# Kernel tuning notes

Measured on AMD Instinct MI355X. Metric: run time of the kernel, lower is better.

The kernel has to match this reference:

```python
import jax, jax.numpy as jnp
import numpy as np

B, S, D, H = 4, 2048, 1024, 16
HD = D // H

def setup_inputs() -> dict:
    key = jax.random.key(0)
    k1, k2, k3 = jax.random.split(key, 3)
    x = jax.random.normal(k1, (B, S, D), dtype=jnp.float32)
    W_qkv = jax.random.normal(k2, (D, 3 * D), dtype=jnp.float32) * (1.0 / np.sqrt(D))
    W_out = jax.random.normal(k3, (D, D), dtype=jnp.float32) * (1.0 / np.sqrt(D))
    causal_mask = jnp.tril(jnp.ones((S, S), dtype=bool))[None, None]  # [1,1,S,S]
    return {"x": x, "causal_mask": causal_mask, "W_qkv": W_qkv, "W_out": W_out}

def reference(x, causal_mask, W_qkv, W_out):
    b, s, d = x.shape
    scale = 1.0 / np.sqrt(HD)
    qkv = x @ W_qkv  # [b,s,3d]
    q, k, v = jnp.split(qkv, 3, axis=-1)
    # [b,h,s,hd]
    q = q.reshape(b, s, H, HD).transpose(0, 2, 1, 3)
    k = k.reshape(b, s, H, HD).transpose(0, 2, 1, 3)
    v = v.reshape(b, s, H, HD).transpose(0, 2, 1, 3)
    scores = jnp.einsum('bhqd,bhkd->bhqk', q, k) * scale
    scores = jnp.where(causal_mask, scores, -jnp.inf)
    attn = jax.nn.softmax(scores, axis=-1)
    out = jnp.einsum('bhqk,bhkd->bhqd', attn, v)
    out = out.transpose(0, 2, 1, 3).reshape(b, s, d)
    return out @ W_out
```

## Files before the change

kernel.cpp:

```cpp
#include <hip/hip_runtime.h>
#include <hip/hip_bf16.h>

typedef __bf16 bf16;
typedef unsigned short u16;
typedef unsigned int u32;
typedef __attribute__((ext_vector_type(8))) __bf16 bf16x8;
typedef __attribute__((ext_vector_type(4))) unsigned short u16x4;
typedef __attribute__((ext_vector_type(4))) float f32x4;

#define B_  4
#define S_  2048
#define D_  1024
#define H_  16
#define HD_ 64

#define QSCALE 0.18033688f

__device__ inline u16 bf16_bits(float f) {
  bf16 h = (bf16)f;
  return __builtin_bit_cast(u16, h);
}

__device__ __forceinline__ void glds16(const bf16* g, bf16* s) {
  __builtin_amdgcn_global_load_lds(
      (const __attribute__((address_space(1))) void*)g,
      (__attribute__((address_space(3))) void*)s, 16, 0, 0);
}

#define MEMFENCE() asm volatile("" ::: "memory")
#define BARRIER_RAW() __builtin_amdgcn_s_barrier()
#define LGKM0() asm volatile("s_waitcnt lgkmcnt(0)" ::: "memory")
#define VMCNT(n) asm volatile("s_waitcnt vmcnt(" #n ")" ::: "memory")

__global__ void cvt_x(const float* __restrict__ in, bf16* __restrict__ out, long n) {
  long i = ((long)blockIdx.x * 256 + threadIdx.x) * 8;
  if (i < n) {
    f32x4 a = *(const f32x4*)(in + i);
    f32x4 b = *(const f32x4*)(in + i + 4);
    bf16x8 v;
#pragma unroll
    for (int j = 0; j < 4; ++j) { v[j] = (bf16)a[j]; v[4 + j] = (bf16)b[j]; }
    *(bf16x8*)(out + i) = v;
  }
}

__global__ void cvt_w(const float* __restrict__ in, bf16* __restrict__ out,
                      int K, int N) {
  __shared__ float tile[32][33];
  int n0 = blockIdx.x * 32, k0 = blockIdx.y * 32;
  int x = threadIdx.x, y = threadIdx.y;
#pragma unroll
  for (int i = 0; i < 32; i += 8)
    tile[y + i][x] = in[(long)(k0 + y + i) * N + (n0 + x)];
  __syncthreads();
#pragma unroll
  for (int i = 0; i < 32; i += 8)
    out[(long)(n0 + y + i) * K + (k0 + x)] = (bf16)tile[x][y + i];
}

template <typename TC>
__launch_bounds__(256)
__global__ void gemm128(const bf16* __restrict__ A, const bf16* __restrict__ Bt,
                        TC* __restrict__ C, int M, int N, int K) {
  __shared__ __attribute__((aligned(16))) bf16 As[8][512];
  __shared__ __attribute__((aligned(16))) bf16 Bs[8][512];
  int t = threadIdx.x;
  int w = t >> 6, lane = t & 63;
  int wr = w >> 1, wc = w & 1;
  int fr = lane & 15, fq = lane >> 4;
  long m0 = (long)blockIdx.y * 128, n0 = (long)blockIdx.x * 128;
  f32x4 acc[4][4] = {};
  const bf16* ag = A  + (m0 + (2 * w) * 16 + fr) * (long)K + fq * 8;
  const bf16* bg = Bt + (n0 + (2 * w) * 16 + fr) * (long)K + fq * 8;
  bf16* al0 = &As[2 * w][0];
  bf16* al1 = &As[2 * w + 1][0];
  bf16* bl0 = &Bs[2 * w][0];
  bf16* bl1 = &Bs[2 * w + 1][0];
  const long K16 = 16 * (long)K;
  for (int k0 = 0; k0 < K; k0 += 32) {
    __syncthreads();
    glds16(ag + k0, al0);
    glds16(ag + k0 + K16, al1);
    glds16(bg + k0, bl0);
    glds16(bg + k0 + K16, bl1);
    __syncthreads();
    bf16x8 af[4], bfv[4];
#pragma unroll
    for (int i = 0; i < 4; ++i) {
      af[i]  = *(const bf16x8*)&As[wr * 4 + i][lane * 8];
      bfv[i] = *(const bf16x8*)&Bs[wc * 4 + i][lane * 8];
    }
#pragma unroll
    for (int mb = 0; mb < 4; ++mb)
#pragma unroll
      for (int nb = 0; nb < 4; ++nb)
        acc[mb][nb] = __builtin_amdgcn_mfma_f32_16x16x32_bf16(
            af[mb], bfv[nb], acc[mb][nb], 0, 0, 0);
  }
#pragma unroll
  for (int mb = 0; mb < 4; ++mb) {
    long row = m0 + wr * 64 + mb * 16 + fq * 4;
#pragma unroll
    for (int nb = 0; nb < 4; ++nb) {
      long col = n0 + wc * 64 + nb * 16 + fr;
#pragma unroll
      for (int i = 0; i < 4; ++i)
        C[(row + i) * (long)N + col] = (TC)acc[mb][nb][i];
    }
  }
}

#define QUAD3(MH, NH)                                                         \
  do {                                                                        \
    _Pragma("unroll") for (int m2 = 0; m2 < 2; ++m2) {                        \
      _Pragma("unroll") for (int n2 = 0; n2 < 3; ++n2) {                      \
        _Pragma("unroll") for (int kc = 0; kc < 2; ++kc)                      \
            acc[(MH) * 2 + m2][(NH) * 3 + n2] =                               \
                __builtin_amdgcn_mfma_f32_16x16x32_bf16(                      \
                    aF[m2][kc], bF[(NH) * 3 + n2][kc],                        \
                    acc[(MH) * 2 + m2][(NH) * 3 + n2], 0, 0, 0);              \
      }                                                                       \
    }                                                                         \
  } while (0)

__launch_bounds__(512, 2)
__global__ void gemm_qkv(const bf16* __restrict__ A, const bf16* __restrict__ Bt,
                         bf16* __restrict__ qk, bf16* __restrict__ vT) {
  __shared__ __attribute__((aligned(16))) bf16 smem[2][32768];
  const int K = 1024;
  int t = threadIdx.x;
  int w = t >> 6, lane = t & 63;
  int wm = w >> 2, wn = w & 3;
  int fr = lane & 15, fq = lane >> 4;
  long m0 = (long)blockIdx.y * 128, n0 = (long)blockIdx.x * 384;

  int o = t * 16;
  int p = o ^ (((o >> 9) & 1) << 5);
  int si = p >> 10;
  int srow = (si >> 1) * 16 + ((p & 1023) >> 6);
  int scol = (si & 1) * 32 + ((p & 63) >> 1);
  const bf16* aS = A  + (m0 + srow) * (long)K + scol;
  const bf16* bS = Bt + (n0 + srow) * (long)K + scol;

  int fro = (fr << 6) + (fq << 4);
  fro ^= (fr & 8) << 2;
  const char* Afr0 = (const char*)&smem[0][0]    + fro;
  const char* Bfr0 = (const char*)&smem[0][8192] + fro;
  bf16* s00 = &smem[0][0];

  f32x4 acc[4][6] = {};
  bf16x8 aF[2][2], bF[6][2];

#define STAGE2(src, dstRegion)                           \
  do {                                                   \
    glds16((src), (dstRegion) + w * 512);                \
    glds16((src) + 65536, (dstRegion) + 4096 + w * 512); \
  } while (0)

  STAGE2(aS,               s00);
  STAGE2(bS,               s00 + 8192);
  STAGE2(bS + 131072,      s00 + 16384);
  STAGE2(bS + 262144,      s00 + 24576);
  STAGE2(aS + 64,          s00 + 32768);
  STAGE2(bS + 64,          s00 + 32768 + 8192);
  STAGE2(bS + 64 + 131072, s00 + 32768 + 16384);
  STAGE2(bS + 64 + 262144, s00 + 32768 + 24576);
  VMCNT(8);
  MEMFENCE(); BARRIER_RAW(); MEMFENCE();

  for (int j = 0; j < 16; ++j) {
    int b = j & 1, nb = b ^ 1;
    long kA = (long)((j + 1 < 16) ? j + 1 : 15) * 64;
    long kB = (long)((j + 2 < 16) ? j + 2 : 15) * 64;
    const char* Ab = Afr0 + b * 65536;
    const char* Bb = Bfr0 + b * 65536;
    bf16* sA = s00 + nb * 32768;
    bf16* sB = s00 + b * 32768 + 8192;

#pragma unroll
    for (int m2 = 0; m2 < 2; ++m2)
#pragma unroll
      for (int kc = 0; kc < 2; ++kc)
        aF[m2][kc] = *(const bf16x8*)(Ab + (4 * wm + m2) * 2048 + kc * 1024);
#pragma unroll
    for (int nf = 0; nf < 3; ++nf)
#pragma unroll
      for (int kc = 0; kc < 2; ++kc)
        bF[nf][kc] = *(const bf16x8*)(Bb + (6 * wn + nf) * 2048 + kc * 1024);
    STAGE2(aS + kA, sA);
    MEMFENCE(); BARRIER_RAW(); LGKM0();
    __builtin_amdgcn_s_setprio(1);
    QUAD3(0, 0);
    __builtin_amdgcn_s_setprio(0);
    MEMFENCE(); BARRIER_RAW(); MEMFENCE();

#pragma unroll
    for (int nf = 3; nf < 6; ++nf)
#pragma unroll
      for (int kc = 0; kc < 2; ++kc)
        bF[nf][kc] = *(const bf16x8*)(Bb + (6 * wn + nf) * 2048 + kc * 1024);
    MEMFENCE(); BARRIER_RAW(); LGKM0();
    __builtin_amdgcn_s_setprio(1);
    QUAD3(0, 1);
    __builtin_amdgcn_s_setprio(0);
    MEMFENCE(); BARRIER_RAW(); MEMFENCE();

#pragma unroll
    for (int m2 = 0; m2 < 2; ++m2)
#pragma unroll
      for (int kc = 0; kc < 2; ++kc)
        aF[m2][kc] = *(const bf16x8*)(Ab + (4 * wm + 2 + m2) * 2048 + kc * 1024);
    STAGE2(bS + kB, sB);
    STAGE2(bS + kB + 131072, sB + 8192);
    MEMFENCE(); BARRIER_RAW(); LGKM0();
    __builtin_amdgcn_s_setprio(1);
    QUAD3(1, 1);
    __builtin_amdgcn_s_setprio(0);
    MEMFENCE(); BARRIER_RAW(); MEMFENCE();

    STAGE2(bS + kB + 262144, sB + 16384);
    MEMFENCE(); BARRIER_RAW(); LGKM0();
    __builtin_amdgcn_s_setprio(1);
    QUAD3(1, 0);
    __builtin_amdgcn_s_setprio(0);
    VMCNT(6);
    MEMFENCE(); BARRIER_RAW(); MEMFENCE();
  }
#undef STAGE2

#pragma unroll
  for (int mf = 0; mf < 4; ++mf) {
    long row = m0 + wm * 64 + mf * 16 + fq * 4;
    long bb = row >> 11;
    long s0r = row & 2047;
#pragma unroll
    for (int nf = 0; nf < 6; ++nf) {
      long col = n0 + wn * 96 + nf * 16 + fr;
      if (col < 2048) {
        float sc = (col < 1024) ? QSCALE : 1.f;
#pragma unroll
        for (int i = 0; i < 4; ++i)
          qk[(row + i) * 2048 + col] = (bf16)(acc[mf][nf][i] * sc);
      } else {
        u16x4 pk;
#pragma unroll
        for (int i = 0; i < 4; ++i) pk[i] = bf16_bits(acc[mf][nf][i]);
        *(u16x4*)(vT + (bb * 1024 + (col - 2048)) * 2048 + s0r) = pk;
      }
    }
  }
}

__launch_bounds__(256, 3)
__global__ void attn_mfma3(const bf16* __restrict__ qk, const bf16* __restrict__ vT,
                           bf16* __restrict__ out) {
  __shared__ __attribute__((aligned(16))) bf16 Ks[2][4][2][512];
  __shared__ __attribute__((aligned(16))) bf16 Vs[2][4][2][512];
  int bx = blockIdx.x;
  int st = 15 - (bx >> 6);
  int hb = bx & 63;
  int h = hb >> 2, b = hb & 3;
  int t = threadIdx.x, w = t >> 6, lane = t & 63;
  int fr = lane & 15, fq = lane >> 4;
  const bf16* qkb = qk + (long)b * S_ * 2048;
  const bf16* vTb = vT + ((long)b * 1024 + h * HD_) * 2048;
  bf16* ob = out + (long)b * S_ * D_ + h * HD_;

  bf16x8 ones;
#pragma unroll
  for (int j = 0; j < 8; ++j) ones[j] = (bf16)1.0f;

  int kappa = 8 * (fr >> 2) + (fr & 3) + 4 * (w & 1) + 32 * (w >> 1);
  const bf16* kg0 = qkb + (long)kappa * 2048 + 1024 + h * HD_ + fq * 8;
  const bf16* vg0 = vTb + (long)(w * 16 + fr) * 2048 + fq * 8;

  int qbase = st * 128 + w * 32;
  int jtmax = 2 * st + 1;

  glds16(kg0,      &Ks[0][w][0][0]);
  glds16(kg0 + 32, &Ks[0][w][1][0]);
  glds16(vg0,      &Vs[0][w][0][0]);
  glds16(vg0 + 32, &Vs[0][w][1][0]);

  bf16x8 aQ[2][2];
#pragma unroll
  for (int s = 0; s < 2; ++s)
#pragma unroll
    for (int kc = 0; kc < 2; ++kc)
      aQ[s][kc] = *(const bf16x8*)(qkb + (long)(qbase + s * 16 + fr) * 2048 +
                                   h * HD_ + kc * 32 + fq * 8);
  f32x4 acc_o[2][4] = {};
  f32x4 acc_l[2] = {};

  for (int jt = 0; jt <= jtmax; ++jt) {
    int c = jt & 1;
    __syncthreads();
    if (jt < jtmax) {
      int n = c ^ 1;
      const bf16* kg = kg0 + (long)(jt + 1) * 64 * 2048;
      const bf16* vg = vg0 + (jt + 1) * 64;
      glds16(kg,      &Ks[n][w][0][0]);
      glds16(kg + 32, &Ks[n][w][1][0]);
      glds16(vg,      &Vs[n][w][0][0]);
      glds16(vg + 32, &Vs[n][w][1][0]);
    }
    bf16x8 bK[4][2], bV[4][2];
#pragma unroll
    for (int nb = 0; nb < 4; ++nb)
#pragma unroll
      for (int kc = 0; kc < 2; ++kc) {
        bK[nb][kc] = *(const bf16x8*)&Ks[c][nb][kc][lane * 8];
        bV[nb][kc] = *(const bf16x8*)&Vs[c][nb][kc][lane * 8];
      }
#pragma unroll
    for (int s = 0; s < 2; ++s) {
      int dlim = qbase + s * 16 - jt * 64;
      if (dlim <= -16) continue;
      f32x4 acc_s[4] = {};
      __builtin_amdgcn_s_setprio(1);
#pragma unroll
      for (int nb = 0; nb < 4; ++nb) {
        acc_s[nb] = __builtin_amdgcn_mfma_f32_16x16x32_bf16(bK[nb][0], aQ[s][0], acc_s[nb], 0, 0, 0);
        acc_s[nb] = __builtin_amdgcn_mfma_f32_16x16x32_bf16(bK[nb][1], aQ[s][1], acc_s[nb], 0, 0, 0);
      }
      __builtin_amdgcn_s_setprio(0);
      float pe[4][4];
      if (dlim < 63) {
        int kbase = 8 * fq;
        int qoff = dlim + fr;
#pragma unroll
        for (int nb = 0; nb < 4; ++nb) {
          int ko = kbase + 4 * (nb & 1) + 32 * (nb >> 1);
#pragma unroll
          for (int i = 0; i < 4; ++i) {
            float pv = exp2f(acc_s[nb][i]);
            pe[nb][i] = (ko + i > qoff) ? 0.f : pv;
          }
        }
      } else {
#pragma unroll
        for (int nb = 0; nb < 4; ++nb)
#pragma unroll
          for (int i = 0; i < 4; ++i) pe[nb][i] = exp2f(acc_s[nb][i]);
      }
      bf16x8 pf[2];
#pragma unroll
      for (int kc = 0; kc < 2; ++kc)
#pragma unroll
        for (int e = 0; e < 8; ++e)
          pf[kc][e] = (bf16)pe[2 * kc + (e >> 2)][e & 3];
      __builtin_amdgcn_s_setprio(1);
#pragma unroll
      for (int kc = 0; kc < 2; ++kc) {
        acc_l[s] = __builtin_amdgcn_mfma_f32_16x16x32_bf16(ones, pf[kc], acc_l[s], 0, 0, 0);
#pragma unroll
        for (int nb = 0; nb < 4; ++nb)
          acc_o[s][nb] = __builtin_amdgcn_mfma_f32_16x16x32_bf16(bV[nb][kc], pf[kc], acc_o[s][nb], 0, 0, 0);
      }
      __builtin_amdgcn_s_setprio(0);
    }
  }
#pragma unroll
  for (int s = 0; s < 2; ++s) {
    float inv = 1.f / acc_l[s][0];
    long q = (long)(qbase + s * 16 + fr);
#pragma unroll
    for (int nb = 0; nb < 4; ++nb) {
      u16x4 pk;
#pragma unroll
      for (int i = 0; i < 4; ++i) pk[i] = bf16_bits(acc_o[s][nb][i] * inv);
      *(u16x4*)(ob + q * D_ + nb * 16 + fq * 4) = pk;
    }
  }
}

__global__ void sentinel_k(float* out, float v, int n) {
  int i = blockIdx.x * 256 + threadIdx.x;
  if (i < n) out[i] = v;
}

extern "C" void kernel_launch(void* const* d_in, const int* in_sizes, int n_in,
                              void* d_out, int out_size, void* d_ws, size_t ws_size,
                              hipStream_t stream) {
  const float* x    = (const float*)d_in[0];
  const float* Wqkv = (const float*)d_in[2];
  const float* Wout = (const float*)d_in[3];
  float* out = (float*)d_out;

  const size_t SD = (size_t)S_ * D_;
  bf16* qk     = (bf16*)d_ws;
  bf16* vT     = qk + (size_t)8192 * 2048;
  bf16* x_bf   = vT + (size_t)4 * 1024 * 2048;
  bf16* ao     = x_bf;
  bf16* wqkv_t = x_bf + (size_t)8192 * 1024;
  bf16* wout_t = wqkv_t + (size_t)3072 * 1024;
  size_t need = ((size_t)16777216 + 8388608 + 8388608 + 3145728 + 1048576) * sizeof(bf16);

  if (ws_size >= need) {
    cvt_x<<<4096, 256, 0, stream>>>(x, x_bf, (long)(B_ * SD));
    cvt_w<<<dim3(3072 / 32, 1024 / 32), dim3(32, 8), 0, stream>>>(Wqkv, wqkv_t, 1024, 3072);
    cvt_w<<<dim3(1024 / 32, 1024 / 32), dim3(32, 8), 0, stream>>>(Wout, wout_t, 1024, 1024);
    gemm_qkv<<<dim3(3072 / 384, (B_ * S_) / 128), 512, 0, stream>>>(
        x_bf, wqkv_t, qk, vT);
    attn_mfma3<<<dim3(1024, 1, 1), 256, 0, stream>>>(qk, vT, ao);
    gemm128<float><<<dim3(D_ / 128, (B_ * S_) / 128), 256, 0, stream>>>(
        ao, wout_t, out, B_ * S_, D_, D_);
  } else {
    float v = 1000.f + (float)(ws_size >> 20);
    int n = (int)((size_t)B_ * SD);
    sentinel_k<<<(n + 255) / 256, 256, 0, stream>>>(out, v, n);
  }
}
```

Before: 264.0 us.

## Replace output projection GEMM with pipelined double-buffered 128x256 kernel

The simple 128x128 output-projection GEMM, which synchronised twice per 32-wide k step, is replaced by a 512-thread kernel. The new kernel uses 128x256 tiles, 64-wide k steps, double-buffered and swizzled LDS, and staggered global-to-LDS prefetch interleaved with MFMA quads under raised wave priority. It mirrors the scheme already used by the QKV GEMM, aiming to hide load latency and raise MFMA utilisation. In exchange it adds more LDS per block and more barriers, and uses a hardcoded K of 1024.

```diff
diff --git a/kernel.cpp b/kernel.cpp
--- a/kernel.cpp
+++ b/kernel.cpp
@@ -56,58 +56,6 @@
 #pragma unroll
   for (int i = 0; i < 32; i += 8)
     out[(long)(n0 + y + i) * K + (k0 + x)] = (bf16)tile[x][y + i];
-}
-
-template <typename TC>
-__launch_bounds__(256)
-__global__ void gemm128(const bf16* __restrict__ A, const bf16* __restrict__ Bt,
-                        TC* __restrict__ C, int M, int N, int K) {
-  __shared__ __attribute__((aligned(16))) bf16 As[8][512];
-  __shared__ __attribute__((aligned(16))) bf16 Bs[8][512];
-  int t = threadIdx.x;
-  int w = t >> 6, lane = t & 63;
-  int wr = w >> 1, wc = w & 1;
-  int fr = lane & 15, fq = lane >> 4;
-  long m0 = (long)blockIdx.y * 128, n0 = (long)blockIdx.x * 128;
-  f32x4 acc[4][4] = {};
-  const bf16* ag = A  + (m0 + (2 * w) * 16 + fr) * (long)K + fq * 8;
-  const bf16* bg = Bt + (n0 + (2 * w) * 16 + fr) * (long)K + fq * 8;
-  bf16* al0 = &As[2 * w][0];
-  bf16* al1 = &As[2 * w + 1][0];
-  bf16* bl0 = &Bs[2 * w][0];
-  bf16* bl1 = &Bs[2 * w + 1][0];
-  const long K16 = 16 * (long)K;
-  for (int k0 = 0; k0 < K; k0 += 32) {
-    __syncthreads();
-    glds16(ag + k0, al0);
-    glds16(ag + k0 + K16, al1);
-    glds16(bg + k0, bl0);
-    glds16(bg + k0 + K16, bl1);
-    __syncthreads();
-    bf16x8 af[4], bfv[4];
-#pragma unroll
-    for (int i = 0; i < 4; ++i) {
-      af[i]  = *(const bf16x8*)&As[wr * 4 + i][lane * 8];
-      bfv[i] = *(const bf16x8*)&Bs[wc * 4 + i][lane * 8];
-    }
-#pragma unroll
-    for (int mb = 0; mb < 4; ++mb)
-#pragma unroll
-      for (int nb = 0; nb < 4; ++nb)
-        acc[mb][nb] = __builtin_amdgcn_mfma_f32_16x16x32_bf16(
-            af[mb], bfv[nb], acc[mb][nb], 0, 0, 0);
-  }
-#pragma unroll
-  for (int mb = 0; mb < 4; ++mb) {
-    long row = m0 + wr * 64 + mb * 16 + fq * 4;
-#pragma unroll
-    for (int nb = 0; nb < 4; ++nb) {
-      long col = n0 + wc * 64 + nb * 16 + fr;
-#pragma unroll
-      for (int i = 0; i < 4; ++i)
-        C[(row + i) * (long)N + col] = (TC)acc[mb][nb][i];
-    }
-  }
 }
 
 #define QUAD3(MH, NH)                                                         \
@@ -247,6 +195,133 @@
         for (int i = 0; i < 4; ++i) pk[i] = bf16_bits(acc[mf][nf][i]);
         *(u16x4*)(vT + (bb * 1024 + (col - 2048)) * 2048 + s0r) = pk;
       }
+    }
+  }
+}
+
+#define QUAD2(MH, NH)                                                         \
+  do {                                                                        \
+    _Pragma("unroll") for (int m2 = 0; m2 < 2; ++m2) {                        \
+      _Pragma("unroll") for (int n2 = 0; n2 < 2; ++n2) {                      \
+        _Pragma("unroll") for (int kc = 0; kc < 2; ++kc)                      \
+            acc[(MH) * 2 + m2][(NH) * 2 + n2] =                               \
+                __builtin_amdgcn_mfma_f32_16x16x32_bf16(                      \
+                    aF[m2][kc], bF[(NH) * 2 + n2][kc],                        \
+                    acc[(MH) * 2 + m2][(NH) * 2 + n2], 0, 0, 0);              \
+      }                                                                       \
+    }                                                                         \
+  } while (0)
+
+__launch_bounds__(512, 2)
+__global__ void gemm_out(const bf16* __restrict__ A, const bf16* __restrict__ Bt,
+                         float* __restrict__ C) {
+  __shared__ __attribute__((aligned(16))) bf16 smem[2][24576];
+  const int K = 1024;
+  int t = threadIdx.x;
+  int w = t >> 6, lane = t & 63;
+  int wm = w >> 2, wn = w & 3;
+  int fr = lane & 15, fq = lane >> 4;
+  long m0 = (long)blockIdx.y * 128, n0 = (long)blockIdx.x * 256;
+
+  int o = t * 16;
+  int p = o ^ (((o >> 9) & 1) << 5);
+  int si = p >> 10;
+  int srow = (si >> 1) * 16 + ((p & 1023) >> 6);
+  int scol = (si & 1) * 32 + ((p & 63) >> 1);
+  const bf16* aS = A  + (m0 + srow) * (long)K + scol;
+  const bf16* bS = Bt + (n0 + srow) * (long)K + scol;
+
+  int fro = (fr << 6) + (fq << 4);
+  fro ^= (fr & 8) << 2;
+  const char* Afr0 = (const char*)&smem[0][0]    + fro;
+  const char* Bfr0 = (const char*)&smem[0][8192] + fro;
+  bf16* s00 = &smem[0][0];
+
+  f32x4 acc[4][4] = {};
+  bf16x8 aF[2][2], bF[4][2];
+
+#define STAGE2(src, dstRegion)                           \
+  do {                                                   \
+    glds16((src), (dstRegion) + w * 512);                \
+    glds16((src) + 65536, (dstRegion) + 4096 + w * 512); \
+  } while (0)
+
+  STAGE2(aS,               s00);
+  STAGE2(bS,               s00 + 8192);
+  STAGE2(bS + 131072,      s00 + 16384);
+  STAGE2(bS + 64,          s00 + 24576 + 8192);
+  STAGE2(bS + 64 + 131072, s00 + 24576 + 16384);
+  VMCNT(4);
+  MEMFENCE(); BARRIER_RAW(); MEMFENCE();
+
+  for (int j = 0; j < 16; ++j) {
+    int b = j & 1, nb = b ^ 1;
+    long kA = (long)((j + 1 < 16) ? j + 1 : 15) * 64;
+    long kB = (long)((j + 2 < 16) ? j + 2 : 15) * 64;
+    const char* Ab = Afr0 + b * 49152;
+    const char* Bb = Bfr0 + b * 49152;
+    bf16* sA = s00 + nb * 24576;
+    bf16* sB = s00 + b * 24576 + 8192;
+
+#pragma unroll
+    for (int m2 = 0; m2 < 2; ++m2)
+#pragma unroll
+      for (int kc = 0; kc < 2; ++kc)
+        aF[m2][kc] = *(const bf16x8*)(Ab + (4 * wm + m2) * 2048 + kc * 1024);
+#pragma unroll
+    for (int nf = 0; nf < 2; ++nf)
+#pragma unroll
+      for (int kc = 0; kc < 2; ++kc)
+        bF[nf][kc] = *(const bf16x8*)(Bb + (4 * wn + nf) * 2048 + kc * 1024);
+    STAGE2(aS + kA, sA);
+    MEMFENCE(); BARRIER_RAW(); LGKM0();
+    __builtin_amdgcn_s_setprio(1);
+    QUAD2(0, 0);
+    __builtin_amdgcn_s_setprio(0);
+    MEMFENCE(); BARRIER_RAW(); MEMFENCE();
+
+#pragma unroll
+    for (int nf = 2; nf < 4; ++nf)
+#pragma unroll
+      for (int kc = 0; kc < 2; ++kc)
+        bF[nf][kc] = *(const bf16x8*)(Bb + (4 * wn + nf) * 2048 + kc * 1024);
+    MEMFENCE(); BARRIER_RAW(); LGKM0();
+    __builtin_amdgcn_s_setprio(1);
+    QUAD2(0, 1);
+    __builtin_amdgcn_s_setprio(0);
+    MEMFENCE(); BARRIER_RAW(); MEMFENCE();
+
+#pragma unroll
+    for (int m2 = 0; m2 < 2; ++m2)
+#pragma unroll
+      for (int kc = 0; kc < 2; ++kc)
+        aF[m2][kc] = *(const bf16x8*)(Ab + (4 * wm + 2 + m2) * 2048 + kc * 1024);
+    STAGE2(bS + kB, sB);
+    MEMFENCE(); BARRIER_RAW(); LGKM0();
+    __builtin_amdgcn_s_setprio(1);
+    QUAD2(1, 1);
+    __builtin_amdgcn_s_setprio(0);
+    MEMFENCE(); BARRIER_RAW(); MEMFENCE();
+
+    STAGE2(bS + kB + 131072, sB + 8192);
+    MEMFENCE(); BARRIER_RAW(); LGKM0();
+    __builtin_amdgcn_s_setprio(1);
+    QUAD2(1, 0);
+    __builtin_amdgcn_s_setprio(0);
+    VMCNT(4);
+    MEMFENCE(); BARRIER_RAW(); MEMFENCE();
+  }
+#undef STAGE2
+
+#pragma unroll
+  for (int mf = 0; mf < 4; ++mf) {
+    long row = m0 + wm * 64 + mf * 16 + fq * 4;
+#pragma unroll
+    for (int nf = 0; nf < 4; ++nf) {
+      long col = n0 + wn * 64 + nf * 16 + fr;
+#pragma unroll
+      for (int i = 0; i < 4; ++i)
+        C[(row + i) * 1024 + col] = acc[mf][nf][i];
     }
   }
 }
@@ -403,8 +478,8 @@
     gemm_qkv<<<dim3(3072 / 384, (B_ * S_) / 128), 512, 0, stream>>>(
         x_bf, wqkv_t, qk, vT);
     attn_mfma3<<<dim3(1024, 1, 1), 256, 0, stream>>>(qk, vT, ao);
-    gemm128<float><<<dim3(D_ / 128, (B_ * S_) / 128), 256, 0, stream>>>(
-        ao, wout_t, out, B_ * S_, D_, D_);
+    gemm_out<<<dim3(1024 / 256, (B_ * S_) / 128), 512, 0, stream>>>(
+        ao, wout_t, out);
   } else {
     float v = 1000.f + (float)(ws_size >> 20);
     int n = (int)((size_t)B_ * SD);
```

Measured after the change: 255.6 us. 3.2% less time.
